# Optimization experiments

Hardware: AMD Instinct MI355X
Metric: run time of the kernel (lower is better)

## Reference

```python
import jax, jax.numpy as jnp
import numpy as np

N_NODES = 50000
N_EDGES = 1600000
NFEAT, NHID, NCLASS = 256, 128, 40
DROPOUT_P = 0.5


def gcn_conv(x, W, b, src, dst, n):
    # PyG GCNConv: h = X W; add self-loops; symmetric norm D^-1/2 (A+I) D^-1/2.
    h = x @ W  # [N, out]
    loop = jnp.arange(n, dtype=src.dtype)
    s = jnp.concatenate([src, loop])  # [E+N]
    d = jnp.concatenate([dst, loop])
    deg = jax.ops.segment_sum(jnp.ones_like(d, dtype=h.dtype), d, num_segments=n)  # in-degree incl. self-loop
    dinv = jax.lax.rsqrt(jnp.maximum(deg, 1.0))
    norm = dinv[s] * dinv[d]  # [E+N]
    msg = h[s] * norm[:, None]  # [E+N, out] gather
    out = jax.ops.segment_sum(msg, d, num_segments=n)  # scatter-add
    return out + b


def setup_inputs() -> dict:
    key = jax.random.key(0)
    k = jax.random.split(key, 7)
    x = jax.random.normal(k[0], (N_NODES, NFEAT), dtype=jnp.float32)
    edge_index = jax.random.randint(k[1], (2, N_EDGES), 0, N_NODES, dtype=jnp.int64)
    W1 = jax.random.normal(k[2], (NFEAT, NHID), dtype=jnp.float32) * (1.0 / np.sqrt(NFEAT))
    b1 = jnp.zeros((NHID,), dtype=jnp.float32)
    W2 = jax.random.normal(k[3], (NHID, NCLASS), dtype=jnp.float32) * (1.0 / np.sqrt(NHID))
    b2 = jnp.zeros((NCLASS,), dtype=jnp.float32)
    keep = jax.random.bernoulli(k[4], 1.0 - DROPOUT_P, (N_NODES, NHID))
    drop_mask = keep.astype(jnp.float32) / (1.0 - DROPOUT_P)  # fixed training-mode dropout mask
    return {"x": x, "edge_index": edge_index, "W1": W1, "b1": b1, "W2": W2, "b2": b2, "drop_mask": drop_mask}


def reference(x, edge_index, W1, b1, W2, b2, drop_mask):
    src, dst = edge_index[0], edge_index[1]
    h = gcn_conv(x, W1, b1, src, dst, N_NODES)
    h = jax.nn.relu(h)
    h = h * drop_mask  # F.dropout(training=True) with fixed mask
    h = gcn_conv(h, W2, b2, src, dst, N_NODES)
    return jax.nn.log_softmax(h, axis=1)
```

## Files before the change

### kernel.cpp

```cpp
#include <hip/hip_runtime.h>
#include <hip/hip_fp16.h>
#include <math.h>

#define N_NODES 50000
#define N_EDGES 1600000
#define NFEAT 256
#define NHID 128
#define NCLASS 40

#define NPAD 50048
#define DUMMY N_NODES

#define BSHIFT 7
#define NBUCK 391
#define CAP 5120
#define EPB 4096

typedef _Float16 f16x8 __attribute__((ext_vector_type(8)));
typedef float f32x4 __attribute__((ext_vector_type(4)));

__global__ __launch_bounds__(256) void k_binA(const int* __restrict__ src,
                                              const int* __restrict__ dst,
                                              int* __restrict__ gcur,
                                              unsigned int* __restrict__ packed) {
    __shared__ int lhist[NBUCK];
    __shared__ int lbase[NBUCK];
    __shared__ int lcur[NBUCK];
    int t = threadIdx.x;
    for (int i = t; i < NBUCK; i += 256) { lhist[i] = 0; lcur[i] = 0; }
    __syncthreads();
    int e0 = blockIdx.x * EPB;
    int e1 = min(e0 + EPB, N_EDGES);
    for (int e = e0 + t; e < e1; e += 256) {
        int b = dst[e] >> BSHIFT;
        atomicAdd(&lhist[b], 1);
    }
    __syncthreads();
    for (int i = t; i < NBUCK; i += 256)
        lbase[i] = atomicAdd(&gcur[i], lhist[i]);
    __syncthreads();
    for (int e = e0 + t; e < e1; e += 256) {
        int d = dst[e];
        int b = d >> BSHIFT;
        int r = atomicAdd(&lcur[b], 1);
        int pos = lbase[b] + r;
        if (pos < CAP)
            packed[(size_t)b * CAP + pos] =
                ((unsigned int)src[e] << BSHIFT) | (unsigned int)(d & 127);
    }
}

__global__ __launch_bounds__(256) void k_binB(const int* __restrict__ gcur,
                                              const unsigned int* __restrict__ packed,
                                              int* __restrict__ esrc,
                                              int* __restrict__ row_beg,
                                              int* __restrict__ row_cnt,
                                              float* __restrict__ dinv) {
    __shared__ unsigned int sp[CAP];
    __shared__ int hist[128];
    __shared__ int scan[128];
    __shared__ int cur[128];
    int b = blockIdx.x;
    int t = threadIdx.x;
    int cnt = min(gcur[b], CAP);
    if (t < 128) { hist[t] = 0; cur[t] = 0; }
    __syncthreads();
    const unsigned int* pin = packed + (size_t)b * CAP;
    for (int i = t; i < cnt; i += 256) {
        unsigned int w = pin[i];
        sp[i] = w;
        atomicAdd(&hist[w & 127], 1);
    }
    __syncthreads();
    if (t == 0) {
        int s = 0;
        for (int i = 0; i < 128; i++) { scan[i] = s; s += hist[i]; }
    }
    __syncthreads();
    for (int i = t; i < cnt; i += 256) {
        unsigned int w = sp[i];
        int dl = (int)(w & 127u);
        int r = atomicAdd(&cur[dl], 1);
        esrc[(size_t)b * CAP + scan[dl] + r] = (int)(w >> BSHIFT);
    }
    if (t < 128) {
        int node = b * 128 + t;
        if (node < N_NODES) {
            row_beg[node] = b * CAP + scan[t];
            row_cnt[node] = hist[t];
            dinv[node] = rsqrtf((float)(hist[t] + 1));
        }
    }
}

__global__ __launch_bounds__(256) void k_prep(const float* __restrict__ W1,
                                              const float* __restrict__ W2,
                                              __half* __restrict__ w1t,
                                              __half* __restrict__ w2t,
                                              int* __restrict__ gcur,
                                              float* __restrict__ dinv) {
    int t = blockIdx.x * 256 + threadIdx.x;
    if (t < NBUCK) gcur[t] = 0;
    if (t < 128 * 256) {
        int n = t >> 8, k = t & 255;
        w1t[t] = __float2half(W1[k * NHID + n]);
    }
    if (t < 48 * 128) {
        int n = t >> 7, k = t & 127;
        w2t[t] = __float2half(n < NCLASS ? W2[k * NCLASS + n] : 0.0f);
    }
    if (t >= N_NODES && t < NPAD) dinv[t] = 0.0f;
}

#define G1_LDA 72
#define G1_LDB 72
#define G1_LDE 136
__global__ __launch_bounds__(256) void k_gemm1(const float* __restrict__ x,
                                               const __half* __restrict__ w1t,
                                               const float* __restrict__ dinv,
                                               __half* __restrict__ h1h) {
    __shared__ __half smem[64 * G1_LDA + 128 * G1_LDB];
    __half* sA = smem;
    __half* sB = smem + 64 * G1_LDA;
    int t = threadIdx.x;
    int rbase = blockIdx.x * 64;
    int lane = t & 63, wv = t >> 6;
    int m = lane & 15, quad = lane >> 4;
    f32x4 acc[8];
    #pragma unroll
    for (int i = 0; i < 8; i++) acc[i] = (f32x4)0.0f;

    int arow = t >> 2, aseg = t & 3;
    int grow = rbase + arow;
    bool avalid = grow < N_NODES;
    int bn = t >> 1, bseg = t & 1;

    for (int k0 = 0; k0 < NFEAT; k0 += 64) {
        const float4* gs = (const float4*)(x + (size_t)grow * NFEAT + k0 + aseg * 16);
        __half* ad = sA + arow * G1_LDA + aseg * 16;
        #pragma unroll
        for (int i = 0; i < 4; i++) {
            float4 v = avalid ? gs[i] : make_float4(0.f, 0.f, 0.f, 0.f);
            __half2 h0 = __float22half2_rn(make_float2(v.x, v.y));
            __half2 h1 = __float22half2_rn(make_float2(v.z, v.w));
            uint2 st;
            st.x = __builtin_bit_cast(unsigned int, h0);
            st.y = __builtin_bit_cast(unsigned int, h1);
            *(uint2*)(ad + i * 4) = st;
        }
        const uint4* ws4 = (const uint4*)(w1t + bn * NFEAT + k0 + bseg * 32);
        uint4* bd = (uint4*)(sB + bn * G1_LDB + bseg * 32);
        #pragma unroll
        for (int i = 0; i < 4; i++) bd[i] = ws4[i];
        __syncthreads();
        #pragma unroll
        for (int kk = 0; kk < 64; kk += 32) {
            f16x8 af = *(const f16x8*)(sA + (wv * 16 + m) * G1_LDA + kk + quad * 8);
            #pragma unroll
            for (int t8 = 0; t8 < 8; t8++) {
                f16x8 bf = *(const f16x8*)(sB + (t8 * 16 + m) * G1_LDB + kk + quad * 8);
                acc[t8] = __builtin_amdgcn_mfma_f32_16x16x32_f16(af, bf, acc[t8], 0, 0, 0);
            }
        }
        __syncthreads();
    }
    float di4[4];
    #pragma unroll
    for (int r = 0; r < 4; r++) di4[r] = dinv[rbase + wv * 16 + quad * 4 + r];
    __half* eb = smem;
    #pragma unroll
    for (int t8 = 0; t8 < 8; t8++) {
        #pragma unroll
        for (int r = 0; r < 4; r++)
            eb[(wv * 16 + quad * 4 + r) * G1_LDE + t8 * 16 + m] = __float2half(acc[t8][r] * di4[r]);
    }
    __syncthreads();
    {
        const uint4* es = (const uint4*)(eb + arow * G1_LDE + aseg * 32);
        uint4* od = (uint4*)(h1h + (size_t)grow * NHID + aseg * 32);
        #pragma unroll
        for (int i = 0; i < 4; i++) od[i] = es[i];
    }
}

#define G2_LDA 136
#define G2_LDB 136
#define G2_LDE 72
__global__ __launch_bounds__(256) void k_gemm2(const __half* __restrict__ h1p,
                                               const __half* __restrict__ w2t,
                                               const float* __restrict__ dinv,
                                               __half* __restrict__ h2p) {
    __shared__ __half smem[64 * G2_LDA + 48 * G2_LDB];
    __half* sA = smem;
    __half* sB = smem + 64 * G2_LDA;
    int t = threadIdx.x;
    int rbase = blockIdx.x * 64;
    int lane = t & 63, wv = t >> 6;
    int m = lane & 15, quad = lane >> 4;
    f32x4 acc[3];
    #pragma unroll
    for (int i = 0; i < 3; i++) acc[i] = (f32x4)0.0f;

    int arow = t >> 2, aseg = t & 3;
    int grow = rbase + arow;
    bool avalid = grow < N_NODES;

    #pragma unroll
    for (int i = 0; i < 3; i++) {
        int idx = t + i * 256;
        int n = idx >> 4, seg = idx & 15;
        *(uint4*)(sB + n * G2_LDB + seg * 8) = *(const uint4*)(w2t + n * NHID + seg * 8);
    }
    {
        const uint4* gs = (const uint4*)(h1p + (size_t)grow * NHID + aseg * 32);
        uint4* ad = (uint4*)(sA + arow * G2_LDA + aseg * 32);
        uint4 z; z.x = z.y = z.z = z.w = 0;
        #pragma unroll
        for (int i = 0; i < 4; i++) ad[i] = avalid ? gs[i] : z;
    }
    __syncthreads();
    #pragma unroll
    for (int kk = 0; kk < 128; kk += 32) {
        f16x8 af = *(const f16x8*)(sA + (wv * 16 + m) * G2_LDA + kk + quad * 8);
        #pragma unroll
        for (int t3 = 0; t3 < 3; t3++) {
            f16x8 bf = *(const f16x8*)(sB + (t3 * 16 + m) * G2_LDB + kk + quad * 8);
            acc[t3] = __builtin_amdgcn_mfma_f32_16x16x32_f16(af, bf, acc[t3], 0, 0, 0);
        }
    }
    __syncthreads();
    float di4[4];
    #pragma unroll
    for (int r = 0; r < 4; r++) di4[r] = dinv[rbase + wv * 16 + quad * 4 + r];
    __half* eb = smem;
    #pragma unroll
    for (int t3 = 0; t3 < 3; t3++) {
        #pragma unroll
        for (int r = 0; r < 4; r++)
            eb[(wv * 16 + quad * 4 + r) * G2_LDE + t3 * 16 + m] = __float2half(acc[t3][r] * di4[r]);
    }
    {
        int zr = t >> 2, zc = 48 + (t & 3) * 4;
        uint2 z; z.x = z.y = 0;
        *(uint2*)(eb + zr * G2_LDE + zc) = z;
    }
    __syncthreads();
    #pragma unroll
    for (int i = 0; i < 2; i++) {
        int idx = t + i * 256;
        int row = idx >> 3, seg = idx & 7;
        int gr = rbase + row;
        *(uint4*)(h2p + (size_t)gr * 64 + seg * 8) = *(const uint4*)(eb + row * G2_LDE + seg * 8);
    }
}

__device__ __forceinline__ void acc8f(float* acc, uint4 v, float d) {
    float2 a0 = __half22float2(__builtin_bit_cast(__half2, v.x));
    float2 a1 = __half22float2(__builtin_bit_cast(__half2, v.y));
    float2 a2 = __half22float2(__builtin_bit_cast(__half2, v.z));
    float2 a3 = __half22float2(__builtin_bit_cast(__half2, v.w));
    acc[0] = fmaf(a0.x, d, acc[0]); acc[1] = fmaf(a0.y, d, acc[1]);
    acc[2] = fmaf(a1.x, d, acc[2]); acc[3] = fmaf(a1.y, d, acc[3]);
    acc[4] = fmaf(a2.x, d, acc[4]); acc[5] = fmaf(a2.y, d, acc[5]);
    acc[6] = fmaf(a3.x, d, acc[6]); acc[7] = fmaf(a3.y, d, acc[7]);
}

__global__ __launch_bounds__(64) void k_agg1(const __half* __restrict__ h1h,
                                             const float* __restrict__ dinv,
                                             const int* __restrict__ row_beg,
                                             const int* __restrict__ row_cnt,
                                             const int* __restrict__ esrc,
                                             const float* __restrict__ b1,
                                             const float* __restrict__ mask,
                                             __half* __restrict__ h1p) {
    int i = blockIdx.x;
    int lane = threadIdx.x;
    int q = lane >> 4;
    int fl = lane & 15;
    const uint4* hv4 = (const uint4*)h1h;
    float di = dinv[i];
    __half2 hacc[4];
    __half2 hz = __half2half2(__float2half(0.0f));
    hacc[0] = hz; hacc[1] = hz; hacc[2] = hz; hacc[3] = hz;
    int s0 = row_beg[i], cnt = row_cnt[i];
    for (int base = 0; base < cnt; base += 64) {
        int idx = base + lane;
        int sv = (idx < cnt) ? esrc[s0 + idx] : DUMMY;
        int n = min(64, cnt - base);
        int nr = (n + 31) & ~31;
        for (int j = 0; j < nr; j += 32) {
            int ss[8]; uint4 vv[8];
            #pragma unroll
            for (int k = 0; k < 8; k++) ss[k] = __shfl(sv, j + 4 * k + q);
            #pragma unroll
            for (int k = 0; k < 8; k++) vv[k] = hv4[(size_t)ss[k] * 16 + fl];
            #pragma unroll
            for (int k = 0; k < 8; k++) {
                hacc[0] = __hadd2(hacc[0], __builtin_bit_cast(__half2, vv[k].x));
                hacc[1] = __hadd2(hacc[1], __builtin_bit_cast(__half2, vv[k].y));
                hacc[2] = __hadd2(hacc[2], __builtin_bit_cast(__half2, vv[k].z));
                hacc[3] = __hadd2(hacc[3], __builtin_bit_cast(__half2, vv[k].w));
            }
        }
    }
    #pragma unroll
    for (int d = 16; d <= 32; d <<= 1) {
        #pragma unroll
        for (int r = 0; r < 4; r++) {
            unsigned int u = __shfl_xor(__builtin_bit_cast(unsigned int, hacc[r]), d);
            hacc[r] = __hadd2(hacc[r], __builtin_bit_cast(__half2, u));
        }
    }
    if (q == 0) {
        float acc[8];
        #pragma unroll
        for (int r = 0; r < 4; r++) {
            float2 f = __half22float2(hacc[r]);
            acc[2 * r] = f.x; acc[2 * r + 1] = f.y;
        }
        uint4 sv4 = hv4[(size_t)i * 16 + fl];
        acc8f(acc, sv4, 1.0f);
        float4 bb0 = ((const float4*)b1)[fl * 2];
        float4 bb1 = ((const float4*)b1)[fl * 2 + 1];
        const float4* mrow = (const float4*)(mask + (size_t)i * NHID);
        float4 mm0 = mrow[fl * 2];
        float4 mm1 = mrow[fl * 2 + 1];
        float o0 = fmaxf(fmaf(acc[0], di, bb0.x), 0.f) * mm0.x;
        float o1 = fmaxf(fmaf(acc[1], di, bb0.y), 0.f) * mm0.y;
        float o2 = fmaxf(fmaf(acc[2], di, bb0.z), 0.f) * mm0.z;
        float o3 = fmaxf(fmaf(acc[3], di, bb0.w), 0.f) * mm0.w;
        float o4 = fmaxf(fmaf(acc[4], di, bb1.x), 0.f) * mm1.x;
        float o5 = fmaxf(fmaf(acc[5], di, bb1.y), 0.f) * mm1.y;
        float o6 = fmaxf(fmaf(acc[6], di, bb1.z), 0.f) * mm1.z;
        float o7 = fmaxf(fmaf(acc[7], di, bb1.w), 0.f) * mm1.w;
        __half2 p0 = __float22half2_rn(make_float2(o0, o1));
        __half2 p1 = __float22half2_rn(make_float2(o2, o3));
        __half2 p2 = __float22half2_rn(make_float2(o4, o5));
        __half2 p3 = __float22half2_rn(make_float2(o6, o7));
        uint4 st;
        st.x = __builtin_bit_cast(unsigned int, p0);
        st.y = __builtin_bit_cast(unsigned int, p1);
        st.z = __builtin_bit_cast(unsigned int, p2);
        st.w = __builtin_bit_cast(unsigned int, p3);
        ((uint4*)h1p)[(size_t)i * 16 + fl] = st;
    }
}

__global__ __launch_bounds__(64) void k_agg2(const __half* __restrict__ h2p,
                                             const float* __restrict__ dinv,
                                             const int* __restrict__ row_beg,
                                             const int* __restrict__ row_cnt,
                                             const int* __restrict__ esrc,
                                             const float* __restrict__ b2,
                                             float* __restrict__ out) {
    int i = blockIdx.x;
    int lane = threadIdx.x;
    int o8 = lane >> 3;
    int fl = lane & 7;
    const uint4* hv4 = (const uint4*)h2p;
    float di = dinv[i];
    __half2 hacc[4];
    __half2 hz = __half2half2(__float2half(0.0f));
    hacc[0] = hz; hacc[1] = hz; hacc[2] = hz; hacc[3] = hz;
    int s0 = row_beg[i], cnt = row_cnt[i];
    for (int base = 0; base < cnt; base += 64) {
        int idx = base + lane;
        int sv = (idx < cnt) ? esrc[s0 + idx] : DUMMY;
        int n = min(64, cnt - base);
        int nr = (n + 31) & ~31;
        for (int j = 0; j < nr; j += 32) {
            int ss[4]; uint4 vv[4];
            #pragma unroll
            for (int k = 0; k < 4; k++) ss[k] = __shfl(sv, j + 8 * k + o8);
            #pragma unroll
            for (int k = 0; k < 4; k++) vv[k] = hv4[(size_t)ss[k] * 8 + fl];
            #pragma unroll
            for (int k = 0; k < 4; k++) {
                hacc[0] = __hadd2(hacc[0], __builtin_bit_cast(__half2, vv[k].x));
                hacc[1] = __hadd2(hacc[1], __builtin_bit_cast(__half2, vv[k].y));
                hacc[2] = __hadd2(hacc[2], __builtin_bit_cast(__half2, vv[k].z));
                hacc[3] = __hadd2(hacc[3], __builtin_bit_cast(__half2, vv[k].w));
            }
        }
    }
    #pragma unroll
    for (int d = 8; d <= 32; d <<= 1) {
        #pragma unroll
        for (int r = 0; r < 4; r++) {
            unsigned int u = __shfl_xor(__builtin_bit_cast(unsigned int, hacc[r]), d);
            hacc[r] = __hadd2(hacc[r], __builtin_bit_cast(__half2, u));
        }
    }
    if (o8 == 0) {
        bool act = (fl < 5);
        float acc[8];
        #pragma unroll
        for (int r = 0; r < 4; r++) {
            float2 f = __half22float2(hacc[r]);
            acc[2 * r] = f.x; acc[2 * r + 1] = f.y;
        }
        uint4 sv4 = hv4[(size_t)i * 8 + fl];
        acc8f(acc, sv4, 1.0f);
        float val[8];
        float m = -INFINITY;
        if (act) {
            float4 bb0 = ((const float4*)b2)[fl * 2];
            float4 bb1 = ((const float4*)b2)[fl * 2 + 1];
            val[0] = fmaf(acc[0], di, bb0.x);
            val[1] = fmaf(acc[1], di, bb0.y);
            val[2] = fmaf(acc[2], di, bb0.z);
            val[3] = fmaf(acc[3], di, bb0.w);
            val[4] = fmaf(acc[4], di, bb1.x);
            val[5] = fmaf(acc[5], di, bb1.y);
            val[6] = fmaf(acc[6], di, bb1.z);
            val[7] = fmaf(acc[7], di, bb1.w);
            #pragma unroll
            for (int k = 0; k < 8; k++) m = fmaxf(m, val[k]);
        }
        m = fmaxf(m, __shfl_xor(m, 1));
        m = fmaxf(m, __shfl_xor(m, 2));
        m = fmaxf(m, __shfl_xor(m, 4));
        float ss = 0.f;
        if (act) {
            #pragma unroll
            for (int k = 0; k < 8; k++) ss += expf(val[k] - m);
        }
        ss += __shfl_xor(ss, 1);
        ss += __shfl_xor(ss, 2);
        ss += __shfl_xor(ss, 4);
        if (act) {
            float ls = m + logf(ss);
            float4 r0 = make_float4(val[0] - ls, val[1] - ls, val[2] - ls, val[3] - ls);
            float4 r1 = make_float4(val[4] - ls, val[5] - ls, val[6] - ls, val[7] - ls);
            float4* orow = (float4*)(out + (size_t)i * NCLASS + fl * 8);
            orow[0] = r0;
            orow[1] = r1;
        }
    }
}

extern "C" void kernel_launch(void* const* d_in, const int* in_sizes, int n_in,
                              void* d_out, int out_size, void* d_ws, size_t ws_size,
                              hipStream_t stream) {
    const float* x    = (const float*)d_in[0];
    const int*   ei   = (const int*)d_in[1];
    const float* W1   = (const float*)d_in[2];
    const float* b1   = (const float*)d_in[3];
    const float* W2   = (const float*)d_in[4];
    const float* b2   = (const float*)d_in[5];
    const float* mask = (const float*)d_in[6];
    float* out = (float*)d_out;

    const int* src = ei;
    const int* dst = ei + N_EDGES;

    char* ws = (char*)d_ws;
    size_t off = 0;
    __half* h1p    = (__half*)(ws + off); off += (size_t)NPAD * NHID * 2;
    __half* h1h    = (__half*)(ws + off); off += (size_t)NPAD * NHID * 2;
    int*    esrc   = (int*)   (ws + off); off += (size_t)NBUCK * CAP * 4 + 256;
    float*  dinv   = (float*) (ws + off); off += 200192;
    int*   row_beg = (int*)   (ws + off); off += 200192;
    int*   row_cnt = (int*)   (ws + off); off += 200192;
    int*   gcur    = (int*)   (ws + off); off += 2048;
    __half* w1t    = (__half*)(ws + off); off += 128 * 256 * 2;
    __half* w2t    = (__half*)(ws + off); off += 48 * 128 * 2;

    unsigned int* packed = (unsigned int*)h1p;
    __half* h2p = h1h;

    k_prep<<<196, 256, 0, stream>>>(W1, W2, w1t, w2t, gcur, dinv);
    k_binA<<<(N_EDGES + EPB - 1) / EPB, 256, 0, stream>>>(src, dst, gcur, packed);
    k_binB<<<NBUCK, 256, 0, stream>>>(gcur, packed, esrc, row_beg, row_cnt, dinv);

    k_gemm1<<<NPAD / 64, 256, 0, stream>>>(x, w1t, dinv, h1h);
    k_agg1<<<N_NODES, 64, 0, stream>>>(h1h, dinv, row_beg, row_cnt, esrc, b1, mask, h1p);
    k_gemm2<<<NPAD / 64, 256, 0, stream>>>(h1p, w2t, dinv, h2p);
    k_agg2<<<N_NODES, 64, 0, stream>>>(h2p, dinv, row_beg, row_cnt, esrc, b2, out);
}
```

Measured before the change: 264.7 us.

## Fuse CSR bucket sort with GEMM1 and split layer-2 features into two planes

Degrees are now counted with global atomics in the binning pass, with a small kernel computing dinv. This lets the second binning stage run in the same launch as the first GEMM, as separate block ranges. The layer-2 hidden output is stored as a 32-wide plane plus an 8-wide plane instead of a zero-padded 64-wide row, so the edge gather in agg2 reads 40 features instead of 64. This trades extra global atomics and one extra tiny launch for fewer bytes gathered and overlap of the sort with the GEMM.

```diff
diff --git a/kernel.cpp b/kernel.cpp
--- a/kernel.cpp
+++ b/kernel.cpp
@@ -22,6 +22,7 @@
 __global__ __launch_bounds__(256) void k_binA(const int* __restrict__ src,
                                               const int* __restrict__ dst,
                                               int* __restrict__ gcur,
+                                              int* __restrict__ deg,
                                               unsigned int* __restrict__ packed) {
     __shared__ int lhist[NBUCK];
     __shared__ int lbase[NBUCK];
@@ -32,8 +33,9 @@
     int e0 = blockIdx.x * EPB;
     int e1 = min(e0 + EPB, N_EDGES);
     for (int e = e0 + t; e < e1; e += 256) {
-        int b = dst[e] >> BSHIFT;
-        atomicAdd(&lhist[b], 1);
+        int d = dst[e];
+        atomicAdd(&lhist[d >> BSHIFT], 1);
+        atomicAdd(&deg[d], 1);
     }
     __syncthreads();
     for (int i = t; i < NBUCK; i += 256)
@@ -50,47 +52,10 @@
     }
 }
 
-__global__ __launch_bounds__(256) void k_binB(const int* __restrict__ gcur,
-                                              const unsigned int* __restrict__ packed,
-                                              int* __restrict__ esrc,
-                                              int* __restrict__ row_beg,
-                                              int* __restrict__ row_cnt,
+__global__ __launch_bounds__(256) void k_dinv(const int* __restrict__ deg,
                                               float* __restrict__ dinv) {
-    __shared__ unsigned int sp[CAP];
-    __shared__ int hist[128];
-    __shared__ int scan[128];
-    __shared__ int cur[128];
-    int b = blockIdx.x;
-    int t = threadIdx.x;
-    int cnt = min(gcur[b], CAP);
-    if (t < 128) { hist[t] = 0; cur[t] = 0; }
-    __syncthreads();
-    const unsigned int* pin = packed + (size_t)b * CAP;
-    for (int i = t; i < cnt; i += 256) {
-        unsigned int w = pin[i];
-        sp[i] = w;
-        atomicAdd(&hist[w & 127], 1);
-    }
-    __syncthreads();
-    if (t == 0) {
-        int s = 0;
-        for (int i = 0; i < 128; i++) { scan[i] = s; s += hist[i]; }
-    }
-    __syncthreads();
-    for (int i = t; i < cnt; i += 256) {
-        unsigned int w = sp[i];
-        int dl = (int)(w & 127u);
-        int r = atomicAdd(&cur[dl], 1);
-        esrc[(size_t)b * CAP + scan[dl] + r] = (int)(w >> BSHIFT);
-    }
-    if (t < 128) {
-        int node = b * 128 + t;
-        if (node < N_NODES) {
-            row_beg[node] = b * CAP + scan[t];
-            row_cnt[node] = hist[t];
-            dinv[node] = rsqrtf((float)(hist[t] + 1));
-        }
-    }
+    int t = blockIdx.x * 256 + threadIdx.x;
+    if (t < NPAD) dinv[t] = (t < N_NODES) ? rsqrtf((float)(deg[t] + 1)) : 0.0f;
 }
 
 __global__ __launch_bounds__(256) void k_prep(const float* __restrict__ W1,
@@ -98,9 +63,10 @@
                                               __half* __restrict__ w1t,
                                               __half* __restrict__ w2t,
                                               int* __restrict__ gcur,
-                                              float* __restrict__ dinv) {
+                                              int* __restrict__ deg) {
     int t = blockIdx.x * 256 + threadIdx.x;
     if (t < NBUCK) gcur[t] = 0;
+    if (t < NPAD) deg[t] = 0;
     if (t < 128 * 256) {
         int n = t >> 8, k = t & 255;
         w1t[t] = __float2half(W1[k * NHID + n]);
@@ -109,77 +75,118 @@
         int n = t >> 7, k = t & 127;
         w2t[t] = __float2half(n < NCLASS ? W2[k * NCLASS + n] : 0.0f);
     }
-    if (t >= N_NODES && t < NPAD) dinv[t] = 0.0f;
 }
 
 #define G1_LDA 72
 #define G1_LDB 72
 #define G1_LDE 136
-__global__ __launch_bounds__(256) void k_gemm1(const float* __restrict__ x,
+#define FUSE_BLOCKS (NBUCK + NPAD / 64)
+__global__ __launch_bounds__(256) void k_fused(const int* __restrict__ gcur,
+                                               const unsigned int* __restrict__ packed,
+                                               int* __restrict__ esrc,
+                                               int* __restrict__ row_beg,
+                                               int* __restrict__ row_cnt,
+                                               const float* __restrict__ x,
                                                const __half* __restrict__ w1t,
                                                const float* __restrict__ dinv,
                                                __half* __restrict__ h1h) {
-    __shared__ __half smem[64 * G1_LDA + 128 * G1_LDB];
-    __half* sA = smem;
-    __half* sB = smem + 64 * G1_LDA;
+    __shared__ __align__(16) char smem[27648];
     int t = threadIdx.x;
-    int rbase = blockIdx.x * 64;
-    int lane = t & 63, wv = t >> 6;
-    int m = lane & 15, quad = lane >> 4;
-    f32x4 acc[8];
-    #pragma unroll
-    for (int i = 0; i < 8; i++) acc[i] = (f32x4)0.0f;
-
-    int arow = t >> 2, aseg = t & 3;
-    int grow = rbase + arow;
-    bool avalid = grow < N_NODES;
-    int bn = t >> 1, bseg = t & 1;
-
-    for (int k0 = 0; k0 < NFEAT; k0 += 64) {
-        const float4* gs = (const float4*)(x + (size_t)grow * NFEAT + k0 + aseg * 16);
-        __half* ad = sA + arow * G1_LDA + aseg * 16;
-        #pragma unroll
-        for (int i = 0; i < 4; i++) {
-            float4 v = avalid ? gs[i] : make_float4(0.f, 0.f, 0.f, 0.f);
-            __half2 h0 = __float22half2_rn(make_float2(v.x, v.y));
-            __half2 h1 = __float22half2_rn(make_float2(v.z, v.w));
-            uint2 st;
-            st.x = __builtin_bit_cast(unsigned int, h0);
-            st.y = __builtin_bit_cast(unsigned int, h1);
-            *(uint2*)(ad + i * 4) = st;
-        }
-        const uint4* ws4 = (const uint4*)(w1t + bn * NFEAT + k0 + bseg * 32);
-        uint4* bd = (uint4*)(sB + bn * G1_LDB + bseg * 32);
-        #pragma unroll
-        for (int i = 0; i < 4; i++) bd[i] = ws4[i];
+    if (blockIdx.x < NBUCK) {
+        unsigned int* sp = (unsigned int*)smem;
+        int* hist = (int*)(smem + 20480);
+        int* scan = (int*)(smem + 20992);
+        int* cur  = (int*)(smem + 21504);
+        int b = blockIdx.x;
+        int cnt = min(gcur[b], CAP);
+        if (t < 128) { hist[t] = 0; cur[t] = 0; }
         __syncthreads();
-        #pragma unroll
-        for (int kk = 0; kk < 64; kk += 32) {
-            f16x8 af = *(const f16x8*)(sA + (wv * 16 + m) * G1_LDA + kk + quad * 8);
-            #pragma unroll
-            for (int t8 = 0; t8 < 8; t8++) {
-                f16x8 bf = *(const f16x8*)(sB + (t8 * 16 + m) * G1_LDB + kk + quad * 8);
-                acc[t8] = __builtin_amdgcn_mfma_f32_16x16x32_f16(af, bf, acc[t8], 0, 0, 0);
+        const unsigned int* pin = packed + (size_t)b * CAP;
+        for (int i = t; i < cnt; i += 256) {
+            unsigned int w = pin[i];
+            sp[i] = w;
+            atomicAdd(&hist[w & 127], 1);
+        }
+        __syncthreads();
+        if (t == 0) {
+            int s = 0;
+            for (int i = 0; i < 128; i++) { scan[i] = s; s += hist[i]; }
+        }
+        __syncthreads();
+        for (int i = t; i < cnt; i += 256) {
+            unsigned int w = sp[i];
+            int dl = (int)(w & 127u);
+            int r = atomicAdd(&cur[dl], 1);
+            esrc[(size_t)b * CAP + scan[dl] + r] = (int)(w >> BSHIFT);
+        }
+        if (t < 128) {
+            int node = b * 128 + t;
+            if (node < N_NODES) {
+                row_beg[node] = b * CAP + scan[t];
+                row_cnt[node] = hist[t];
             }
         }
+    } else {
+        __half* sA = (__half*)smem;
+        __half* sB = (__half*)(smem) + 64 * G1_LDA;
+        int rbase = (blockIdx.x - NBUCK) * 64;
+        int lane = t & 63, wv = t >> 6;
+        int m = lane & 15, quad = lane >> 4;
+        f32x4 acc[8];
+        #pragma unroll
+        for (int i = 0; i < 8; i++) acc[i] = (f32x4)0.0f;
+
+        int arow = t >> 2, aseg = t & 3;
+        int grow = rbase + arow;
+        bool avalid = grow < N_NODES;
+        int bn = t >> 1, bseg = t & 1;
+
+        for (int k0 = 0; k0 < NFEAT; k0 += 64) {
+            const float4* gs = (const float4*)(x + (size_t)grow * NFEAT + k0 + aseg * 16);
+            __half* ad = sA + arow * G1_LDA + aseg * 16;
+            #pragma unroll
+            for (int i = 0; i < 4; i++) {
+                float4 v = avalid ? gs[i] : make_float4(0.f, 0.f, 0.f, 0.f);
+                __half2 h0 = __float22half2_rn(make_float2(v.x, v.y));
+                __half2 h1 = __float22half2_rn(make_float2(v.z, v.w));
+                uint2 st;
+                st.x = __builtin_bit_cast(unsigned int, h0);
+                st.y = __builtin_bit_cast(unsigned int, h1);
+                *(uint2*)(ad + i * 4) = st;
+            }
+            const uint4* ws4 = (const uint4*)(w1t + bn * NFEAT + k0 + bseg * 32);
+            uint4* bd = (uint4*)(sB + bn * G1_LDB + bseg * 32);
+            #pragma unroll
+            for (int i = 0; i < 4; i++) bd[i] = ws4[i];
+            __syncthreads();
+            #pragma unroll
+            for (int kk = 0; kk < 64; kk += 32) {
+                f16x8 af = *(const f16x8*)(sA + (wv * 16 + m) * G1_LDA + kk + quad * 8);
+                #pragma unroll
+                for (int t8 = 0; t8 < 8; t8++) {
+                    f16x8 bf = *(const f16x8*)(sB + (t8 * 16 + m) * G1_LDB + kk + quad * 8);
+                    acc[t8] = __builtin_amdgcn_mfma_f32_16x16x32_f16(af, bf, acc[t8], 0, 0, 0);
+                }
+            }
+            __syncthreads();
+        }
+        float di4[4];
+        #pragma unroll
+        for (int r = 0; r < 4; r++) di4[r] = dinv[rbase + wv * 16 + quad * 4 + r];
+        __half* eb = (__half*)smem;
+        #pragma unroll
+        for (int t8 = 0; t8 < 8; t8++) {
+            #pragma unroll
+            for (int r = 0; r < 4; r++)
+                eb[(wv * 16 + quad * 4 + r) * G1_LDE + t8 * 16 + m] = __float2half(acc[t8][r] * di4[r]);
+        }
         __syncthreads();
-    }
-    float di4[4];
-    #pragma unroll
-    for (int r = 0; r < 4; r++) di4[r] = dinv[rbase + wv * 16 + quad * 4 + r];
-    __half* eb = smem;
-    #pragma unroll
-    for (int t8 = 0; t8 < 8; t8++) {
-        #pragma unroll
-        for (int r = 0; r < 4; r++)
-            eb[(wv * 16 + quad * 4 + r) * G1_LDE + t8 * 16 + m] = __float2half(acc[t8][r] * di4[r]);
-    }
-    __syncthreads();
-    {
-        const uint4* es = (const uint4*)(eb + arow * G1_LDE + aseg * 32);
-        uint4* od = (uint4*)(h1h + (size_t)grow * NHID + aseg * 32);
-        #pragma unroll
-        for (int i = 0; i < 4; i++) od[i] = es[i];
+        {
+            const uint4* es = (const uint4*)(eb + arow * G1_LDE + aseg * 32);
+            uint4* od = (uint4*)(h1h + (size_t)grow * NHID + aseg * 32);
+            #pragma unroll
+            for (int i = 0; i < 4; i++) od[i] = es[i];
+        }
     }
 }
 
@@ -189,7 +196,7 @@
 __global__ __launch_bounds__(256) void k_gemm2(const __half* __restrict__ h1p,
                                                const __half* __restrict__ w2t,
                                                const float* __restrict__ dinv,
-                                               __half* __restrict__ h2p) {
+                                               __half* __restrict__ h2pl) {
     __shared__ __half smem[64 * G2_LDA + 48 * G2_LDB];
     __half* sA = smem;
     __half* sB = smem + 64 * G2_LDA;
@@ -239,18 +246,19 @@
         for (int r = 0; r < 4; r++)
             eb[(wv * 16 + quad * 4 + r) * G2_LDE + t3 * 16 + m] = __float2half(acc[t3][r] * di4[r]);
     }
-    {
-        int zr = t >> 2, zc = 48 + (t & 3) * 4;
-        uint2 z; z.x = z.y = 0;
-        *(uint2*)(eb + zr * G2_LDE + zc) = z;
-    }
     __syncthreads();
+    __half* pA = h2pl;
+    __half* pB = h2pl + (size_t)NPAD * 32;
     #pragma unroll
     for (int i = 0; i < 2; i++) {
         int idx = t + i * 256;
         int row = idx >> 3, seg = idx & 7;
         int gr = rbase + row;
-        *(uint4*)(h2p + (size_t)gr * 64 + seg * 8) = *(const uint4*)(eb + row * G2_LDE + seg * 8);
+        if (seg <= 4) {
+            uint4 v = *(const uint4*)(eb + row * G2_LDE + seg * 8);
+            if (seg < 4) ((uint4*)pA)[(size_t)gr * 4 + seg] = v;
+            else        ((uint4*)pB)[gr] = v;
+        }
     }
 }
 
@@ -346,7 +354,7 @@
     }
 }
 
-__global__ __launch_bounds__(64) void k_agg2(const __half* __restrict__ h2p,
+__global__ __launch_bounds__(64) void k_agg2(const __half* __restrict__ h2pl,
                                              const float* __restrict__ dinv,
                                              const int* __restrict__ row_beg,
                                              const int* __restrict__ row_cnt,
@@ -355,86 +363,128 @@
                                              float* __restrict__ out) {
     int i = blockIdx.x;
     int lane = threadIdx.x;
-    int o8 = lane >> 3;
-    int fl = lane & 7;
-    const uint4* hv4 = (const uint4*)h2p;
+    int g = lane >> 2;
+    int fl = lane & 3;
+    const uint4* pA = (const uint4*)h2pl;
+    const uint4* pB = (const uint4*)(h2pl + (size_t)NPAD * 32);
     float di = dinv[i];
-    __half2 hacc[4];
+    __half2 a0[4], a1[4];
     __half2 hz = __half2half2(__float2half(0.0f));
-    hacc[0] = hz; hacc[1] = hz; hacc[2] = hz; hacc[3] = hz;
+    #pragma unroll
+    for (int r = 0; r < 4; r++) { a0[r] = hz; a1[r] = hz; }
     int s0 = row_beg[i], cnt = row_cnt[i];
     for (int base = 0; base < cnt; base += 64) {
         int idx = base + lane;
         int sv = (idx < cnt) ? esrc[s0 + idx] : DUMMY;
+        uint4 v1 = pB[sv];
+        a1[0] = __hadd2(a1[0], __builtin_bit_cast(__half2, v1.x));
+        a1[1] = __hadd2(a1[1], __builtin_bit_cast(__half2, v1.y));
+        a1[2] = __hadd2(a1[2], __builtin_bit_cast(__half2, v1.z));
+        a1[3] = __hadd2(a1[3], __builtin_bit_cast(__half2, v1.w));
         int n = min(64, cnt - base);
         int nr = (n + 31) & ~31;
         for (int j = 0; j < nr; j += 32) {
-            int ss[4]; uint4 vv[4];
-            #pragma unroll
-            for (int k = 0; k < 4; k++) ss[k] = __shfl(sv, j + 8 * k + o8);
-            #pragma unroll
-            for (int k = 0; k < 4; k++) vv[k] = hv4[(size_t)ss[k] * 8 + fl];
-            #pragma unroll
-            for (int k = 0; k < 4; k++) {
-                hacc[0] = __hadd2(hacc[0], __builtin_bit_cast(__half2, vv[k].x));
-                hacc[1] = __hadd2(hacc[1], __builtin_bit_cast(__half2, vv[k].y));
-                hacc[2] = __hadd2(hacc[2], __builtin_bit_cast(__half2, vv[k].z));
-                hacc[3] = __hadd2(hacc[3], __builtin_bit_cast(__half2, vv[k].w));
+            int ss[2]; uint4 vv[2];
+            #pragma unroll
+            for (int k = 0; k < 2; k++) ss[k] = __shfl(sv, j + 16 * k + g);
+            #pragma unroll
+            for (int k = 0; k < 2; k++) vv[k] = pA[(size_t)ss[k] * 4 + fl];
+            #pragma unroll
+            for (int k = 0; k < 2; k++) {
+                a0[0] = __hadd2(a0[0], __builtin_bit_cast(__half2, vv[k].x));
+                a0[1] = __hadd2(a0[1], __builtin_bit_cast(__half2, vv[k].y));
+                a0[2] = __hadd2(a0[2], __builtin_bit_cast(__half2, vv[k].z));
+                a0[3] = __hadd2(a0[3], __builtin_bit_cast(__half2, vv[k].w));
             }
         }
     }
     #pragma unroll
-    for (int d = 8; d <= 32; d <<= 1) {
+    for (int d = 1; d <= 32; d <<= 1) {
         #pragma unroll
         for (int r = 0; r < 4; r++) {
-            unsigned int u = __shfl_xor(__builtin_bit_cast(unsigned int, hacc[r]), d);
-            hacc[r] = __hadd2(hacc[r], __builtin_bit_cast(__half2, u));
-        }
-    }
-    if (o8 == 0) {
-        bool act = (fl < 5);
+            unsigned int u = __shfl_xor(__builtin_bit_cast(unsigned int, a1[r]), d);
+            a1[r] = __hadd2(a1[r], __builtin_bit_cast(__half2, u));
+            if (d >= 4) {
+                unsigned int u0 = __shfl_xor(__builtin_bit_cast(unsigned int, a0[r]), d);
+                a0[r] = __hadd2(a0[r], __builtin_bit_cast(__half2, u0));
+            }
+        }
+    }
+    float val0[8], val1[8];
+    if (g == 0) {
         float acc[8];
         #pragma unroll
         for (int r = 0; r < 4; r++) {
-            float2 f = __half22float2(hacc[r]);
+            float2 f = __half22float2(a0[r]);
             acc[2 * r] = f.x; acc[2 * r + 1] = f.y;
         }
-        uint4 sv4 = hv4[(size_t)i * 8 + fl];
-        acc8f(acc, sv4, 1.0f);
-        float val[8];
-        float m = -INFINITY;
-        if (act) {
-            float4 bb0 = ((const float4*)b2)[fl * 2];
-            float4 bb1 = ((const float4*)b2)[fl * 2 + 1];
-            val[0] = fmaf(acc[0], di, bb0.x);
-            val[1] = fmaf(acc[1], di, bb0.y);
-            val[2] = fmaf(acc[2], di, bb0.z);
-            val[3] = fmaf(acc[3], di, bb0.w);
-            val[4] = fmaf(acc[4], di, bb1.x);
-            val[5] = fmaf(acc[5], di, bb1.y);
-            val[6] = fmaf(acc[6], di, bb1.z);
-            val[7] = fmaf(acc[7], di, bb1.w);
-            #pragma unroll
-            for (int k = 0; k < 8; k++) m = fmaxf(m, val[k]);
-        }
-        m = fmaxf(m, __shfl_xor(m, 1));
-        m = fmaxf(m, __shfl_xor(m, 2));
-        m = fmaxf(m, __shfl_xor(m, 4));
-        float ss = 0.f;
-        if (act) {
-            #pragma unroll
-            for (int k = 0; k < 8; k++) ss += expf(val[k] - m);
-        }
-        ss += __shfl_xor(ss, 1);
-        ss += __shfl_xor(ss, 2);
-        ss += __shfl_xor(ss, 4);
-        if (act) {
-            float ls = m + logf(ss);
-            float4 r0 = make_float4(val[0] - ls, val[1] - ls, val[2] - ls, val[3] - ls);
-            float4 r1 = make_float4(val[4] - ls, val[5] - ls, val[6] - ls, val[7] - ls);
-            float4* orow = (float4*)(out + (size_t)i * NCLASS + fl * 8);
-            orow[0] = r0;
-            orow[1] = r1;
+        uint4 s4 = pA[(size_t)i * 4 + fl];
+        acc8f(acc, s4, 1.0f);
+        float4 bb0 = *(const float4*)(b2 + fl * 8);
+        float4 bb1 = *(const float4*)(b2 + fl * 8 + 4);
+        val0[0] = fmaf(acc[0], di, bb0.x);
+        val0[1] = fmaf(acc[1], di, bb0.y);
+        val0[2] = fmaf(acc[2], di, bb0.z);
+        val0[3] = fmaf(acc[3], di, bb0.w);
+        val0[4] = fmaf(acc[4], di, bb1.x);
+        val0[5] = fmaf(acc[5], di, bb1.y);
+        val0[6] = fmaf(acc[6], di, bb1.z);
+        val0[7] = fmaf(acc[7], di, bb1.w);
+    }
+    if (lane == 0) {
+        float acc[8];
+        #pragma unroll
+        for (int r = 0; r < 4; r++) {
+            float2 f = __half22float2(a1[r]);
+            acc[2 * r] = f.x; acc[2 * r + 1] = f.y;
+        }
+        acc8f(acc, pB[i], 1.0f);
+        float4 bb0 = *(const float4*)(b2 + 32);
+        float4 bb1 = *(const float4*)(b2 + 36);
+        val1[0] = fmaf(acc[0], di, bb0.x);
+        val1[1] = fmaf(acc[1], di, bb0.y);
+        val1[2] = fmaf(acc[2], di, bb0.z);
+        val1[3] = fmaf(acc[3], di, bb0.w);
+        val1[4] = fmaf(acc[4], di, bb1.x);
+        val1[5] = fmaf(acc[5], di, bb1.y);
+        val1[6] = fmaf(acc[6], di, bb1.z);
+        val1[7] = fmaf(acc[7], di, bb1.w);
+    }
+    float m = -INFINITY;
+    if (g == 0) {
+        #pragma unroll
+        for (int k = 0; k < 8; k++) m = fmaxf(m, val0[k]);
+    }
+    if (lane == 0) {
+        #pragma unroll
+        for (int k = 0; k < 8; k++) m = fmaxf(m, val1[k]);
+    }
+    m = fmaxf(m, __shfl_xor(m, 1));
+    m = fmaxf(m, __shfl_xor(m, 2));
+    float ssum = 0.f;
+    if (g == 0) {
+        #pragma unroll
+        for (int k = 0; k < 8; k++) ssum += expf(val0[k] - m);
+    }
+    if (lane == 0) {
+        #pragma unroll
+        for (int k = 0; k < 8; k++) ssum += expf(val1[k] - m);
+    }
+    ssum += __shfl_xor(ssum, 1);
+    ssum += __shfl_xor(ssum, 2);
+    if (g == 0) {
+        float ls = m + logf(ssum);
+        float4 r0 = make_float4(val0[0] - ls, val0[1] - ls, val0[2] - ls, val0[3] - ls);
+        float4 r1 = make_float4(val0[4] - ls, val0[5] - ls, val0[6] - ls, val0[7] - ls);
+        float4* orow = (float4*)(out + (size_t)i * NCLASS + fl * 8);
+        orow[0] = r0;
+        orow[1] = r1;
+        if (lane == 0) {
+            float4 r2 = make_float4(val1[0] - ls, val1[1] - ls, val1[2] - ls, val1[3] - ls);
+            float4 r3 = make_float4(val1[4] - ls, val1[5] - ls, val1[6] - ls, val1[7] - ls);
+            float4* orow1 = (float4*)(out + (size_t)i * NCLASS + 32);
+            orow1[0] = r2;
+            orow1[1] = r3;
         }
     }
 }
@@ -459,22 +509,23 @@
     __half* h1p    = (__half*)(ws + off); off += (size_t)NPAD * NHID * 2;
     __half* h1h    = (__half*)(ws + off); off += (size_t)NPAD * NHID * 2;
     int*    esrc   = (int*)   (ws + off); off += (size_t)NBUCK * CAP * 4 + 256;
-    float*  dinv   = (float*) (ws + off); off += 200192;
-    int*   row_beg = (int*)   (ws + off); off += 200192;
-    int*   row_cnt = (int*)   (ws + off); off += 200192;
-    int*   gcur    = (int*)   (ws + off); off += 2048;
+    int*    deg    = (int*)   (ws + off); off += (size_t)NPAD * 4;
+    float*  dinv   = (float*) (ws + off); off += (size_t)NPAD * 4;
+    int*   row_beg = (int*)   (ws + off); off += (size_t)NPAD * 4;
+    int*   row_cnt = (int*)   (ws + off); off += (size_t)NPAD * 4;
+    int*    gcur   = (int*)   (ws + off); off += 2048;
     __half* w1t    = (__half*)(ws + off); off += 128 * 256 * 2;
     __half* w2t    = (__half*)(ws + off); off += 48 * 128 * 2;
 
     unsigned int* packed = (unsigned int*)h1p;
-    __half* h2p = h1h;
-
-    k_prep<<<196, 256, 0, stream>>>(W1, W2, w1t, w2t, gcur, dinv);
-    k_binA<<<(N_EDGES + EPB - 1) / EPB, 256, 0, stream>>>(src, dst, gcur, packed);
-    k_binB<<<NBUCK, 256, 0, stream>>>(gcur, packed, esrc, row_beg, row_cnt, dinv);
-
-    k_gemm1<<<NPAD / 64, 256, 0, stream>>>(x, w1t, dinv, h1h);
+    __half* h2pl = h1h;
+
+    k_prep<<<196, 256, 0, stream>>>(W1, W2, w1t, w2t, gcur, deg);
+    k_binA<<<(N_EDGES + EPB - 1) / EPB, 256, 0, stream>>>(src, dst, gcur, deg, packed);
+    k_dinv<<<196, 256, 0, stream>>>(deg, dinv);
+    k_fused<<<FUSE_BLOCKS, 256, 0, stream>>>(gcur, packed, esrc, row_beg, row_cnt,
+                                             x, w1t, dinv, h1h);
     k_agg1<<<N_NODES, 64, 0, stream>>>(h1h, dinv, row_beg, row_cnt, esrc, b1, mask, h1p);
-    k_gemm2<<<NPAD / 64, 256, 0, stream>>>(h1p, w2t, dinv, h2p);
-    k_agg2<<<N_NODES, 64, 0, stream>>>(h2p, dinv, row_beg, row_cnt, esrc, b2, out);
-}
+    k_gemm2<<<NPAD / 64, 256, 0, stream>>>(h1p, w2t, dinv, h2pl);
+    k_agg2<<<N_NODES, 64, 0, stream>>>(h2pl, dinv, row_beg, row_cnt, esrc, b2, out);
+}
```

After: 326.4 us. 23.3% more time.
